# Performance work log

Measured on AMD Instinct MI355X. Metric: run time of the kernel, lower is better.

## Reference

```python
import jax, jax.numpy as jnp
import numpy as np
from jax import lax

N_NODES = 16384
N_EDGES = 262144
T = 64
F_IN = 8
H1, C1 = 12, 16          # globals H and O in the source
HID2 = H1 * C1           # 192, input to second GATConv
LSTM_H = 128
TRAIN_LEN = 32
TARGET_ID = 0
NEG_SLOPE = 0.2


def setup_inputs() -> dict:
    key = jax.random.key(0)
    ks = jax.random.split(key, 16)
    x = jax.random.normal(ks[0], (T, N_NODES, F_IN), jnp.float32)
    src = jax.random.randint(ks[1], (T, N_EDGES), 0, N_NODES)
    dst = jax.random.randint(ks[2], (T, N_EDGES), 0, N_NODES)
    dst = jnp.where(dst == src, (dst + 1) % N_NODES, dst)  # guarantee no self-loops
    edge_index = jnp.stack([src, dst], axis=1)  # (T, 2, E)
    g = lambda k, sh: jax.random.normal(k, sh, jnp.float32) * 0.1
    return {
        "x": x, "edge_index": edge_index,
        "Wl1": g(ks[3], (F_IN, H1 * C1)),
        "att_l1": g(ks[4], (1, H1, C1)), "att_r1": g(ks[5], (1, H1, C1)),
        "b1": jnp.zeros((H1 * C1,), jnp.float32),
        "Wl2": g(ks[6], (HID2, 1)),
        "att_l2": g(ks[7], (1, 1, 1)), "att_r2": g(ks[8], (1, 1, 1)),
        "b2": jnp.zeros((1,), jnp.float32),
        "Wih0": g(ks[9], (4 * LSTM_H, 1)), "Whh0": g(ks[10], (4 * LSTM_H, LSTM_H)),
        "bih0": jnp.zeros((4 * LSTM_H,), jnp.float32), "bhh0": jnp.zeros((4 * LSTM_H,), jnp.float32),
        "Wih1": g(ks[11], (4 * LSTM_H, LSTM_H)), "Whh1": g(ks[12], (4 * LSTM_H, LSTM_H)),
        "bih1": jnp.zeros((4 * LSTM_H,), jnp.float32), "bhh1": jnp.zeros((4 * LSTM_H,), jnp.float32),
        "Wlin": g(ks[13], (1, LSTM_H)), "blin": jnp.zeros((1,), jnp.float32),
    }


def _gat(x, ei, W, att_l, att_r, b, heads, outc, concat):
    N = x.shape[0]
    xl = (x @ W).reshape(N, heads, outc)              # (N,H,C)
    al = jnp.sum(xl * att_l, axis=-1)                 # (N,H)
    ar = jnp.sum(xl * att_r, axis=-1)                 # (N,H)
    loop = jnp.arange(N)
    src = jnp.concatenate([ei[0], loop])              # add self loops (inputs have none)
    dst = jnp.concatenate([ei[1], loop])
    alpha = jax.nn.leaky_relu(al[src] + ar[dst], NEG_SLOPE)  # (E+N, H)
    # segment softmax over destination neighborhoods
    amax = jax.ops.segment_max(alpha, dst, num_segments=N)
    ex = jnp.exp(alpha - amax[dst])
    alpha = ex / (jax.ops.segment_sum(ex, dst, num_segments=N)[dst] + 1e-16)
    # hardcoded per-edge-row edits from message(): s and v copies, then blend
    s = alpha.at[jnp.array([1, 2, 12, 19, 22])].set(0.0).at[jnp.array([7, 14])].set(1.0)
    v = alpha.at[jnp.array([10, 13])].set(0.5).at[jnp.array([17])].set(0.0)
    alpha = 0.8 * alpha + 0.1 * s + 0.1 * v
    out = jax.ops.segment_sum(xl[src] * alpha[:, :, None], dst, num_segments=N)  # (N,H,C)
    out = out.reshape(N, heads * outc) if concat else out.mean(axis=1)
    return out + b


def _lstm_layer(xs, Wih, Whh, bih, bhh):
    # xs: (L, B, in) -> hs: (L, B, H); torch gate order i,f,g,o
    Bsz, Hd = xs.shape[1], Whh.shape[1]
    def step(carry, xt):
        h, c = carry
        gates = xt @ Wih.T + h @ Whh.T + bih + bhh
        i, f, g, o = jnp.split(gates, 4, axis=-1)
        c = jax.nn.sigmoid(f) * c + jax.nn.sigmoid(i) * jnp.tanh(g)
        h = jax.nn.sigmoid(o) * jnp.tanh(c)
        return (h, c), h
    init = (jnp.zeros((Bsz, Hd), xs.dtype), jnp.zeros((Bsz, Hd), xs.dtype))
    _, hs = lax.scan(step, init, xs)
    return hs


def reference(x, edge_index, Wl1, att_l1, att_r1, b1, Wl2, att_l2, att_r2, b2,
              Wih0, Whh0, bih0, bhh0, Wih1, Whh1, bih1, bhh1, Wlin, blin):
    def per_t(args):
        xt, eit = args
        h = _gat(xt, eit, Wl1, att_l1, att_r1, b1, H1, C1, True)
        h = jax.nn.elu(h)
        h = _gat(h, eit, Wl2, att_l2, att_r2, b2, 1, 1, False)
        return h[:, 0]
    out = lax.map(per_t, (x, edge_index))             # (T, N) == xs_out
    series = lax.stop_gradient(out[:, TARGET_ID])     # split_sequences detaches
    idx = jnp.arange(T - TRAIN_LEN)[:, None] + jnp.arange(TRAIN_LEN)[None, :]
    ts = series[idx][:, :, None]                      # (B, L, 1), batch_first
    xs = jnp.transpose(ts, (1, 0, 2))                 # (L, B, 1)
    hs = _lstm_layer(xs, Wih0, Whh0, bih0, bhh0)
    hs = _lstm_layer(hs, Wih1, Whh1, bih1, bhh1)
    return hs[-1] @ Wlin.T + blin                     # (B, 1)
```

## Files before the change

### kernel.cpp

```cpp
#include <hip/hip_runtime.h>
#include <math.h>

#define T 64
#define NN 16384
#define NE 262144
#define FIN 8
#define H1H 12
#define C1C 16
#define HID 192
#define CAP2 95
#define SCAP 96
#define DEGCAP 127
#define LH 128
#define G4 512
#define NB 32
#define NL 32

#define DEV __device__ __forceinline__

DEV float wave_max(float v){
  #pragma unroll
  for (int m = 32; m; m >>= 1) v = fmaxf(v, __shfl_xor(v, m));
  return v;
}
DEV float wave_sum(float v){
  #pragma unroll
  for (int m = 32; m; m >>= 1) v += __shfl_xor(v, m);
  return v;
}
DEV float leaky(float x){ return x >= 0.f ? x : 0.2f * x; }
DEV float sigmoidf(float x){ return 1.f / (1.f + expf(-x)); }

DEV float apply_edit(float a, int eid){
  if (eid >= 32) return a;
  const unsigned m09 = (1u<<1)|(1u<<2)|(1u<<7)|(1u<<10)|(1u<<12)|(1u<<13)|(1u<<14)|(1u<<17)|(1u<<19)|(1u<<22);
  const unsigned mp1 = (1u<<7)|(1u<<14);
  const unsigned mp05 = (1u<<10)|(1u<<13);
  unsigned b = 1u << eid;
  float r = (m09 & b) ? 0.9f * a : a;
  if (mp1 & b) r += 0.1f;
  if (mp05 & b) r += 0.05f;
  return r;
}

__global__ __launch_bounds__(256) void k_scan0(const int* __restrict__ ei,
                                               int* __restrict__ cnt2, int* __restrict__ list2){
  long long gid = (long long)blockIdx.x * blockDim.x + threadIdx.x;
  long long e4 = gid * 4;
  int t = (int)(e4 >> 18);
  int e = (int)(e4 & (NE - 1));
  const int* dstp = ei + (size_t)t * 2 * NE + NE + e;
  int4 d = *(const int4*)dstp;
  int dd[4] = {d.x, d.y, d.z, d.w};
  #pragma unroll
  for (int q = 0; q < 4; q++){
    if (dd[q] == 0){
      int pos = atomicAdd(&cnt2[t], 1);
      if (pos < CAP2) list2[t * CAP2 + pos] = e + q;
    }
  }
}

__global__ __launch_bounds__(128) void k_build(const int* __restrict__ ei, const int* __restrict__ cnt2,
                                               const int* __restrict__ list2, int* __restrict__ scnt,
                                               int* __restrict__ Slist, int* __restrict__ slot_of){
  int t = blockIdx.x;
  int* so = slot_of + (size_t)t * NN;
  int m = min(cnt2[t], CAP2);
  for (int i = threadIdx.x; i < m + 1; i += blockDim.x){
    int u = (i == m) ? 0 : ei[(size_t)t * 2 * NE + list2[t * CAP2 + i]];
    int old = atomicCAS(&so[u], -1, -2);
    if (old == -1){
      int s = atomicAdd(&scnt[t], 1);
      Slist[t * SCAP + s] = u;
      __hip_atomic_store(&so[u], s, __ATOMIC_RELAXED, __HIP_MEMORY_SCOPE_AGENT);
    }
  }
}

__global__ __launch_bounds__(256) void k_scan1(const int* __restrict__ ei, const int* __restrict__ slot_of,
                                               int* __restrict__ ecnt1, int* __restrict__ elist1){
  long long gid = (long long)blockIdx.x * blockDim.x + threadIdx.x;
  long long e4 = gid * 4;
  int t = (int)(e4 >> 18);
  int e = (int)(e4 & (NE - 1));
  const int* dstp = ei + (size_t)t * 2 * NE + NE + e;
  int4 d = *(const int4*)dstp;
  int dd[4] = {d.x, d.y, d.z, d.w};
  #pragma unroll
  for (int q = 0; q < 4; q++){
    int sl = slot_of[(size_t)t * NN + dd[q]];
    if (sl >= 0){
      int pos = atomicAdd(&ecnt1[t * SCAP + sl], 1);
      if (pos < DEGCAP) elist1[((size_t)t * SCAP + sl) * DEGCAP + pos] = e + q;
    }
  }
}

__global__ __launch_bounds__(64, 4) void k_gat1(const float* __restrict__ x, const int* __restrict__ ei,
                                             const float* __restrict__ Wl1, const float* __restrict__ attl,
                                             const float* __restrict__ attr, const float* __restrict__ b1,
                                             const int* __restrict__ scnt, const int* __restrict__ Slist,
                                             const int* __restrict__ ecnt1, const int* __restrict__ elist1,
                                             float* __restrict__ h1){
  int t = blockIdx.y, s = blockIdx.x, h = blockIdx.z;
  if (s >= scnt[t]) return;
  int lane = threadIdx.x;
  int u = Slist[t * SCAP + s];
  int deg = min(ecnt1[t * SCAP + s], DEGCAP);
  int tot = deg + 1;
  bool two = tot > 64;
  const float* xt = x + (size_t)t * NN * FIN;
  const int* srcp = ei + (size_t)t * 2 * NE;
  const int* el = elist1 + ((size_t)t * SCAP + s) * DEGCAP;

  float4 xu_a = ((const float4*)(xt + (size_t)u * FIN))[0];
  float4 xu_b = ((const float4*)(xt + (size_t)u * FIN))[1];
  float xu[FIN] = {xu_a.x, xu_a.y, xu_a.z, xu_a.w, xu_b.x, xu_b.y, xu_b.z, xu_b.w};

  bool act0 = lane < tot;
  int eid0 = 1 << 29;
  int su0 = u;
  if (lane < deg){ int e = el[lane]; eid0 = e; su0 = srcp[e]; }
  float4 xs0a = ((const float4*)(xt + (size_t)su0 * FIN))[0];
  float4 xs0b = ((const float4*)(xt + (size_t)su0 * FIN))[1];
  float xsrc0[FIN] = {xs0a.x, xs0a.y, xs0a.z, xs0a.w, xs0b.x, xs0b.y, xs0b.z, xs0b.w};

  bool act1 = false; int eid1 = 1 << 29;
  float xsrc1[FIN];
  if (two){
    int idx = 64 + lane;
    act1 = idx < tot;
    int su1 = u;
    if (idx < deg){ int e = el[idx]; eid1 = e; su1 = srcp[e]; }
    float4 xs1a = ((const float4*)(xt + (size_t)su1 * FIN))[0];
    float4 xs1b = ((const float4*)(xt + (size_t)su1 * FIN))[1];
    #pragma unroll
    for (int f = 0; f < 4; f++) xsrc1[f] = (&xs1a.x)[f];
    #pragma unroll
    for (int f = 0; f < 4; f++) xsrc1[4 + f] = (&xs1b.x)[f];
  }

  const float* Wh = Wl1 + h * C1C;
  const float* attlh = attl + h * C1C;
  const float* attrh = attr + h * C1C;

  float ar = 0.f;
  #pragma unroll
  for (int c = 0; c < C1C; c++){
    float v = 0.f;
    #pragma unroll
    for (int f = 0; f < FIN; f++) v = fmaf(xu[f], Wh[f * HID + c], v);
    ar = fmaf(v, attrh[c], ar);
  }

  float xls0[C1C];
  float al0 = 0.f;
  #pragma unroll
  for (int c = 0; c < C1C; c++){
    float v = 0.f;
    #pragma unroll
    for (int f = 0; f < FIN; f++) v = fmaf(xsrc0[f], Wh[f * HID + c], v);
    xls0[c] = v;
    al0 = fmaf(v, attlh[c], al0);
  }
  float raw0 = act0 ? leaky(al0 + ar) : -INFINITY;

  float xls1[C1C];
  float raw1 = -INFINITY;
  if (two){
    float al1 = 0.f;
    #pragma unroll
    for (int c = 0; c < C1C; c++){
      float v = 0.f;
      #pragma unroll
      for (int f = 0; f < FIN; f++) v = fmaf(xsrc1[f], Wh[f * HID + c], v);
      xls1[c] = v;
      al1 = fmaf(v, attlh[c], al1);
    }
    raw1 = act1 ? leaky(al1 + ar) : -INFINITY;
  }

  float M = wave_max(fmaxf(raw0, raw1));
  float ex0 = act0 ? expf(raw0 - M) : 0.f;
  float ex1 = act1 ? expf(raw1 - M) : 0.f;
  float S = wave_sum(ex0 + ex1);
  float den = S + 1e-16f;
  float alpha0 = apply_edit(ex0 / den, eid0);
  float alpha1 = two ? apply_edit(ex1 / den, eid1) : 0.f;

  float sum[C1C];
  #pragma unroll
  for (int c = 0; c < C1C; c++){
    sum[c] = xls0[c] * alpha0;
    if (two) sum[c] = fmaf(xls1[c], alpha1, sum[c]);
  }
  #pragma unroll
  for (int m = 32; m; m >>= 1){
    #pragma unroll
    for (int c = 0; c < C1C; c++) sum[c] += __shfl_xor(sum[c], m);
  }
  if (lane == 0){
    float* h1p = h1 + ((size_t)t * SCAP + s) * HID + h * C1C;
    #pragma unroll
    for (int c = 0; c < C1C; c++){
      float v = sum[c] + b1[h * C1C + c];
      h1p[c] = v > 0.f ? v : expm1f(v);
    }
  }
}

__global__ __launch_bounds__(64) void k_gat2(const int* __restrict__ ei, const float* __restrict__ Wl2,
                                             const float* __restrict__ attl2_, const float* __restrict__ attr2_,
                                             const float* __restrict__ b2, const int* __restrict__ cnt2,
                                             const int* __restrict__ list2, const int* __restrict__ slot_of,
                                             const float* __restrict__ h1, float* __restrict__ series){
  int t = blockIdx.x; int lane = threadIdx.x;
  int deg = min(cnt2[t], CAP2);
  int tot = deg + 1;
  const int* srcp = ei + (size_t)t * 2 * NE;
  const int* so = slot_of + (size_t)t * NN;
  float attl2 = attl2_[0], attr2 = attr2_[0];
  int sl0 = so[0];
  const float* h1t = h1 + (size_t)t * SCAP * HID;

  float x0 = 0.f;
  for (int k = 0; k < HID; k++) x0 += h1t[(size_t)sl0 * HID + k] * Wl2[k];

  bool act[2]; int eid[2]; float xl2[2];
  #pragma unroll
  for (int ch = 0; ch < 2; ch++){
    int idx = ch * 64 + lane;
    act[ch] = idx < tot;
    eid[ch] = 1 << 29;
    int sl = sl0;
    if (idx < deg){ int e = list2[t * CAP2 + idx]; eid[ch] = e; sl = so[srcp[e]]; }
    float v = 0.f;
    if (act[ch]) for (int k = 0; k < HID; k++) v += h1t[(size_t)sl * HID + k] * Wl2[k];
    xl2[ch] = v;
  }
  float raw[2];
  #pragma unroll
  for (int ch = 0; ch < 2; ch++) raw[ch] = act[ch] ? leaky(attl2 * xl2[ch] + attr2 * x0) : -INFINITY;
  float M = wave_max(fmaxf(raw[0], raw[1]));
  float ex[2];
  #pragma unroll
  for (int ch = 0; ch < 2; ch++) ex[ch] = act[ch] ? expf(raw[ch] - M) : 0.f;
  float S = wave_sum(ex[0] + ex[1]);
  float den = S + 1e-16f;
  float contrib = apply_edit(ex[0] / den, eid[0]) * xl2[0] + apply_edit(ex[1] / den, eid[1]) * xl2[1];
  contrib = wave_sum(contrib);
  if (lane == 0) series[t] = contrib + b2[0];
}

#define AT_LOADR(p)    __hip_atomic_load((p), __ATOMIC_RELAXED, __HIP_MEMORY_SCOPE_AGENT)
#define AT_STORER(p,v) __hip_atomic_store((p), (v), __ATOMIC_RELAXED, __HIP_MEMORY_SCOPE_AGENT)

#define REP32(M) M(0)M(1)M(2)M(3)M(4)M(5)M(6)M(7)M(8)M(9)M(10)M(11)M(12)M(13)M(14)M(15)\
                 M(16)M(17)M(18)M(19)M(20)M(21)M(22)M(23)M(24)M(25)M(26)M(27)M(28)M(29)M(30)M(31)
#define WDECL(i) float4 w##i;
#define WLOAD(i) w##i = Wr[i];
#define WPIN(i)  asm volatile("" : "+v"(w##i.x), "+v"(w##i.y), "+v"(w##i.z), "+v"(w##i.w));
#define WFMA(i)  { float4 hv = h4[i]; a0 = fmaf(w##i.x, hv.x, a0); a1 = fmaf(w##i.y, hv.y, a1); \
                   a2 = fmaf(w##i.z, hv.z, a2); a3 = fmaf(w##i.w, hv.w, a3); }

__global__ __launch_bounds__(512, 2) void k_lstm(const float* __restrict__ series,
    const float* __restrict__ Wih0, const float* __restrict__ Whh0,
    const float* __restrict__ bih0, const float* __restrict__ bhh0,
    const float* __restrict__ Wih1, const float* __restrict__ Whh1,
    const float* __restrict__ bih1, const float* __restrict__ bhh1,
    const float* __restrict__ Wlin, const float* __restrict__ blin,
    float* __restrict__ h0g, float* __restrict__ xpart,
    int* __restrict__ flagA, int* __restrict__ flagB, float* __restrict__ out){
  int j = threadIdx.x;
  int st = blockIdx.x >> 5;
  int b = blockIdx.x & 31;
  __shared__ __align__(16) float h_lds[LH];
  __shared__ __align__(16) float c_lds[LH];
  __shared__ float gate_lds[G4];
  __shared__ float s_series[NL];
  __shared__ int rdy_lds;
  const float4* h4 = (const float4*)h_lds;

  if (st == 0){
    const float4* Wr = (const float4*)(Whh0 + (size_t)j * LH);
    REP32(WDECL)
    REP32(WLOAD)
    REP32(WPIN)
    float wih = Wih0[j];
    float bsum = bih0[j] + bhh0[j];
    if (j < LH){ h_lds[j] = 0.f; c_lds[j] = 0.f; }
    if (j < NL) s_series[j] = series[b + j];
    __syncthreads();
    for (int t = 0; t < NL; t++){
      float a0 = 0.f, a1 = 0.f, a2 = 0.f, a3 = 0.f;
      REP32(WFMA)
      float acc = fmaf(wih, s_series[t], bsum) + (a0 + a1) + (a2 + a3);
      gate_lds[j] = acc;
      __syncthreads();
      if (j < LH){
        float ig = sigmoidf(gate_lds[j]);
        float fg = sigmoidf(gate_lds[LH + j]);
        float gg = tanhf(gate_lds[2 * LH + j]);
        float og = sigmoidf(gate_lds[3 * LH + j]);
        float c = fg * c_lds[j] + ig * gg;
        float h = og * tanhf(c);
        c_lds[j] = c; h_lds[j] = h;
        AT_STORER(&h0g[(b * NL + t) * LH + j], h);
      }
      __syncthreads();
      if (j == 0) AT_STORER(&flagA[b], t + 1);
    }
  } else if (st == 1){
    const float4* Wr = (const float4*)(Wih1 + (size_t)j * LH);
    REP32(WDECL)
    REP32(WLOAD)
    REP32(WPIN)
    int ready = 0;
    for (int t = 0; t < NL; t++){
      if (ready <= t){
        if (j == 0){
          int f;
          while ((f = AT_LOADR(&flagA[b])) < t + 1) __builtin_amdgcn_s_sleep(1);
          rdy_lds = f;
        }
        __syncthreads();
        ready = rdy_lds;
      }
      if (j < LH) h_lds[j] = AT_LOADR(&h0g[(b * NL + t) * LH + j]);
      __syncthreads();
      float a0 = 0.f, a1 = 0.f, a2 = 0.f, a3 = 0.f;
      REP32(WFMA)
      AT_STORER(&xpart[(b * NL + t) * G4 + j], (a0 + a1) + (a2 + a3));
      __syncthreads();
      if (j == 0) AT_STORER(&flagB[b], t + 1);
    }
  } else {
    const float4* Wr = (const float4*)(Whh1 + (size_t)j * LH);
    REP32(WDECL)
    REP32(WLOAD)
    REP32(WPIN)
    float bsum = bih1[j] + bhh1[j];
    if (j < LH){ h_lds[j] = 0.f; c_lds[j] = 0.f; }
    __syncthreads();
    int ready = 0;
    for (int t = 0; t < NL; t++){
      if (ready <= t){
        if (j == 0){
          int f;
          while ((f = AT_LOADR(&flagB[b])) < t + 1) __builtin_amdgcn_s_sleep(1);
          rdy_lds = f;
        }
        __syncthreads();
        ready = rdy_lds;
      }
      float xj = AT_LOADR(&xpart[(b * NL + t) * G4 + j]);
      float a0 = 0.f, a1 = 0.f, a2 = 0.f, a3 = 0.f;
      REP32(WFMA)
      float acc = xj + bsum + (a0 + a1) + (a2 + a3);
      gate_lds[j] = acc;
      __syncthreads();
      if (j < LH){
        float ig = sigmoidf(gate_lds[j]);
        float fg = sigmoidf(gate_lds[LH + j]);
        float gg = tanhf(gate_lds[2 * LH + j]);
        float og = sigmoidf(gate_lds[3 * LH + j]);
        float c = fg * c_lds[j] + ig * gg;
        float h = og * tanhf(c);
        c_lds[j] = c; h_lds[j] = h;
      }
      __syncthreads();
    }
    if (j == 0){
      float s2 = blin[0];
      for (int k = 0; k < LH; k++) s2 += Wlin[k] * h_lds[k];
      out[b] = s2;
    }
  }
}

extern "C" void kernel_launch(void* const* d_in, const int* in_sizes, int n_in,
                              void* d_out, int out_size, void* d_ws, size_t ws_size,
                              hipStream_t stream) {
  const float* x     = (const float*)d_in[0];
  const int*   ei    = (const int*)  d_in[1];
  const float* Wl1   = (const float*)d_in[2];
  const float* attl1 = (const float*)d_in[3];
  const float* attr1 = (const float*)d_in[4];
  const float* b1    = (const float*)d_in[5];
  const float* Wl2   = (const float*)d_in[6];
  const float* attl2 = (const float*)d_in[7];
  const float* attr2 = (const float*)d_in[8];
  const float* b2    = (const float*)d_in[9];
  const float* Wih0  = (const float*)d_in[10];
  const float* Whh0  = (const float*)d_in[11];
  const float* bih0  = (const float*)d_in[12];
  const float* bhh0  = (const float*)d_in[13];
  const float* Wih1  = (const float*)d_in[14];
  const float* Whh1  = (const float*)d_in[15];
  const float* bih1  = (const float*)d_in[16];
  const float* bhh1  = (const float*)d_in[17];
  const float* Wlin  = (const float*)d_in[18];
  const float* blin  = (const float*)d_in[19];
  float* out = (float*)d_out;

  char* wsb = (char*)d_ws;
  size_t off = 0;
  auto alloc = [&](size_t bytes)->void*{
    void* p = wsb + off;
    off += (bytes + 255) & ~(size_t)255;
    return p;
  };
  int* cnt2  = (int*)alloc(T * 4);
  int* scnt  = (int*)alloc(T * 4);
  int* ecnt1 = (int*)alloc(T * SCAP * 4);
  int* flagA = (int*)alloc(NB * 4);
  int* flagB = (int*)alloc(NB * 4);
  size_t ctrl_bytes = off;
  int* slot_of = (int*)alloc((size_t)T * NN * 4);
  int* list2   = (int*)alloc((size_t)T * CAP2 * 4);
  int* Slist   = (int*)alloc((size_t)T * SCAP * 4);
  int* elist1  = (int*)alloc((size_t)T * SCAP * DEGCAP * 4);
  float* h1    = (float*)alloc((size_t)T * SCAP * HID * 4);
  float* series= (float*)alloc(T * 4);
  float* h0g   = (float*)alloc((size_t)NB * NL * LH * 4);
  float* xpart = (float*)alloc((size_t)NB * NL * G4 * 4);

  hipMemsetAsync(d_ws, 0, ctrl_bytes, stream);
  hipMemsetAsync(slot_of, 0xFF, (size_t)T * NN * 4, stream);

  k_scan0<<<T * NE / 4 / 256, 256, 0, stream>>>(ei, cnt2, list2);
  k_build<<<T, 128, 0, stream>>>(ei, cnt2, list2, scnt, Slist, slot_of);
  k_scan1<<<T * NE / 4 / 256, 256, 0, stream>>>(ei, slot_of, ecnt1, elist1);
  k_gat1<<<dim3(SCAP, T, H1H), 64, 0, stream>>>(x, ei, Wl1, attl1, attr1, b1, scnt, Slist, ecnt1, elist1, h1);
  k_gat2<<<T, 64, 0, stream>>>(ei, Wl2, attl2, attr2, b2, cnt2, list2, slot_of, h1, series);
  k_lstm<<<96, 512, 0, stream>>>(series, Wih0, Whh0, bih0, bhh0, Wih1, Whh1, bih1, bhh1,
                                 Wlin, blin, h0g, xpart, flagA, flagB, out);
}
```

Before: 415.7 us.

## Split LSTM gate dot products across two thread halves with LDS reduction

The LSTM kernel now launches 1024 threads per block instead of 512. Each gate row's 128-long dot product is split between two threads that each hold half the weights in registers, and the two partial sums are reduced through shared memory. This halves the serial FMA chain and the register pressure per thread. In exchange it adds an extra barrier and LDS round trip per timestep, and the flag polling no longer caches readiness ahead of time.

```diff
diff --git a/kernel.cpp b/kernel.cpp
--- a/kernel.cpp
+++ b/kernel.cpp
@@ -256,15 +256,14 @@
 #define AT_LOADR(p)    __hip_atomic_load((p), __ATOMIC_RELAXED, __HIP_MEMORY_SCOPE_AGENT)
 #define AT_STORER(p,v) __hip_atomic_store((p), (v), __ATOMIC_RELAXED, __HIP_MEMORY_SCOPE_AGENT)
 
-#define REP32(M) M(0)M(1)M(2)M(3)M(4)M(5)M(6)M(7)M(8)M(9)M(10)M(11)M(12)M(13)M(14)M(15)\
-                 M(16)M(17)M(18)M(19)M(20)M(21)M(22)M(23)M(24)M(25)M(26)M(27)M(28)M(29)M(30)M(31)
+#define REP16(M) M(0)M(1)M(2)M(3)M(4)M(5)M(6)M(7)M(8)M(9)M(10)M(11)M(12)M(13)M(14)M(15)
 #define WDECL(i) float4 w##i;
 #define WLOAD(i) w##i = Wr[i];
 #define WPIN(i)  asm volatile("" : "+v"(w##i.x), "+v"(w##i.y), "+v"(w##i.z), "+v"(w##i.w));
-#define WFMA(i)  { float4 hv = h4[i]; a0 = fmaf(w##i.x, hv.x, a0); a1 = fmaf(w##i.y, hv.y, a1); \
+#define WFMA(i)  { float4 hv = h4h[i]; a0 = fmaf(w##i.x, hv.x, a0); a1 = fmaf(w##i.y, hv.y, a1); \
                    a2 = fmaf(w##i.z, hv.z, a2); a3 = fmaf(w##i.w, hv.w, a3); }
 
-__global__ __launch_bounds__(512, 2) void k_lstm(const float* __restrict__ series,
+__global__ __launch_bounds__(1024, 4) void k_lstm(const float* __restrict__ series,
     const float* __restrict__ Wih0, const float* __restrict__ Whh0,
     const float* __restrict__ bih0, const float* __restrict__ bhh0,
     const float* __restrict__ Wih1, const float* __restrict__ Whh1,
@@ -272,106 +271,102 @@
     const float* __restrict__ Wlin, const float* __restrict__ blin,
     float* __restrict__ h0g, float* __restrict__ xpart,
     int* __restrict__ flagA, int* __restrict__ flagB, float* __restrict__ out){
-  int j = threadIdx.x;
+  int tid = threadIdx.x;
   int st = blockIdx.x >> 5;
   int b = blockIdx.x & 31;
+  int row = tid & 511;
+  int half = tid >> 9;
   __shared__ __align__(16) float h_lds[LH];
-  __shared__ __align__(16) float c_lds[LH];
-  __shared__ float gate_lds[G4];
+  __shared__ float c_lds[LH];
+  __shared__ float part[1024];
   __shared__ float s_series[NL];
-  __shared__ int rdy_lds;
   const float4* h4 = (const float4*)h_lds;
 
   if (st == 0){
-    const float4* Wr = (const float4*)(Whh0 + (size_t)j * LH);
-    REP32(WDECL)
-    REP32(WLOAD)
-    REP32(WPIN)
-    float wih = Wih0[j];
-    float bsum = bih0[j] + bhh0[j];
-    if (j < LH){ h_lds[j] = 0.f; c_lds[j] = 0.f; }
-    if (j < NL) s_series[j] = series[b + j];
+    const float4* Wr = (const float4*)(Whh0 + (size_t)row * LH) + half * 16;
+    REP16(WDECL)
+    REP16(WLOAD)
+    REP16(WPIN)
+    float wih = Wih0[row];
+    float bsum = bih0[row] + bhh0[row];
+    if (tid < LH){ h_lds[tid] = 0.f; c_lds[tid] = 0.f; }
+    if (tid < NL) s_series[tid] = series[b + tid];
     __syncthreads();
     for (int t = 0; t < NL; t++){
+      const float4* h4h = h4 + half * 16;
       float a0 = 0.f, a1 = 0.f, a2 = 0.f, a3 = 0.f;
-      REP32(WFMA)
-      float acc = fmaf(wih, s_series[t], bsum) + (a0 + a1) + (a2 + a3);
-      gate_lds[j] = acc;
-      __syncthreads();
-      if (j < LH){
-        float ig = sigmoidf(gate_lds[j]);
-        float fg = sigmoidf(gate_lds[LH + j]);
-        float gg = tanhf(gate_lds[2 * LH + j]);
-        float og = sigmoidf(gate_lds[3 * LH + j]);
-        float c = fg * c_lds[j] + ig * gg;
+      REP16(WFMA)
+      part[tid] = (a0 + a1) + (a2 + a3);
+      __syncthreads();
+      if (tid < G4) part[tid] = part[tid] + part[tid + G4] + fmaf(wih, s_series[t], bsum);
+      __syncthreads();
+      if (tid < LH){
+        float ig = sigmoidf(part[tid]);
+        float fg = sigmoidf(part[LH + tid]);
+        float gg = tanhf(part[2 * LH + tid]);
+        float og = sigmoidf(part[3 * LH + tid]);
+        float c = fg * c_lds[tid] + ig * gg;
         float h = og * tanhf(c);
-        c_lds[j] = c; h_lds[j] = h;
-        AT_STORER(&h0g[(b * NL + t) * LH + j], h);
+        c_lds[tid] = c; h_lds[tid] = h;
+        AT_STORER(&h0g[(b * NL + t) * LH + tid], h);
       }
       __syncthreads();
-      if (j == 0) AT_STORER(&flagA[b], t + 1);
+      if (tid == 0) AT_STORER(&flagA[b], t + 1);
     }
   } else if (st == 1){
-    const float4* Wr = (const float4*)(Wih1 + (size_t)j * LH);
-    REP32(WDECL)
-    REP32(WLOAD)
-    REP32(WPIN)
-    int ready = 0;
+    const float4* Wr = (const float4*)(Wih1 + (size_t)row * LH) + half * 16;
+    REP16(WDECL)
+    REP16(WLOAD)
+    REP16(WPIN)
     for (int t = 0; t < NL; t++){
-      if (ready <= t){
-        if (j == 0){
-          int f;
-          while ((f = AT_LOADR(&flagA[b])) < t + 1) __builtin_amdgcn_s_sleep(1);
-          rdy_lds = f;
-        }
-        __syncthreads();
-        ready = rdy_lds;
+      if (tid == 0){
+        while (AT_LOADR(&flagA[b]) < t + 1) __builtin_amdgcn_s_sleep(1);
       }
-      if (j < LH) h_lds[j] = AT_LOADR(&h0g[(b * NL + t) * LH + j]);
-      __syncthreads();
+      __syncthreads();
+      if (tid < LH) h_lds[tid] = AT_LOADR(&h0g[(b * NL + t) * LH + tid]);
+      __syncthreads();
+      const float4* h4h = h4 + half * 16;
       float a0 = 0.f, a1 = 0.f, a2 = 0.f, a3 = 0.f;
-      REP32(WFMA)
-      AT_STORER(&xpart[(b * NL + t) * G4 + j], (a0 + a1) + (a2 + a3));
-      __syncthreads();
-      if (j == 0) AT_STORER(&flagB[b], t + 1);
+      REP16(WFMA)
+      part[tid] = (a0 + a1) + (a2 + a3);
+      __syncthreads();
+      if (tid < G4) AT_STORER(&xpart[(b * NL + t) * G4 + tid], part[tid] + part[tid + G4]);
+      __syncthreads();
+      if (tid == 0) AT_STORER(&flagB[b], t + 1);
     }
   } else {
-    const float4* Wr = (const float4*)(Whh1 + (size_t)j * LH);
-    REP32(WDECL)
-    REP32(WLOAD)
-    REP32(WPIN)
-    float bsum = bih1[j] + bhh1[j];
-    if (j < LH){ h_lds[j] = 0.f; c_lds[j] = 0.f; }
+    const float4* Wr = (const float4*)(Whh1 + (size_t)row * LH) + half * 16;
+    REP16(WDECL)
+    REP16(WLOAD)
+    REP16(WPIN)
+    float bsum = bih1[row] + bhh1[row];
+    if (tid < LH){ h_lds[tid] = 0.f; c_lds[tid] = 0.f; }
     __syncthreads();
-    int ready = 0;
     for (int t = 0; t < NL; t++){
-      if (ready <= t){
-        if (j == 0){
-          int f;
-          while ((f = AT_LOADR(&flagB[b])) < t + 1) __builtin_amdgcn_s_sleep(1);
-          rdy_lds = f;
-        }
-        __syncthreads();
-        ready = rdy_lds;
+      if (tid == 0){
+        while (AT_LOADR(&flagB[b]) < t + 1) __builtin_amdgcn_s_sleep(1);
       }
-      float xj = AT_LOADR(&xpart[(b * NL + t) * G4 + j]);
+      __syncthreads();
+      const float4* h4h = h4 + half * 16;
       float a0 = 0.f, a1 = 0.f, a2 = 0.f, a3 = 0.f;
-      REP32(WFMA)
-      float acc = xj + bsum + (a0 + a1) + (a2 + a3);
-      gate_lds[j] = acc;
-      __syncthreads();
-      if (j < LH){
-        float ig = sigmoidf(gate_lds[j]);
-        float fg = sigmoidf(gate_lds[LH + j]);
-        float gg = tanhf(gate_lds[2 * LH + j]);
-        float og = sigmoidf(gate_lds[3 * LH + j]);
-        float c = fg * c_lds[j] + ig * gg;
+      REP16(WFMA)
+      float xj = (tid < G4) ? AT_LOADR(&xpart[(b * NL + t) * G4 + tid]) : 0.f;
+      part[tid] = (a0 + a1) + (a2 + a3);
+      __syncthreads();
+      if (tid < G4) part[tid] = part[tid] + part[tid + G4] + xj + bsum;
+      __syncthreads();
+      if (tid < LH){
+        float ig = sigmoidf(part[tid]);
+        float fg = sigmoidf(part[LH + tid]);
+        float gg = tanhf(part[2 * LH + tid]);
+        float og = sigmoidf(part[3 * LH + tid]);
+        float c = fg * c_lds[tid] + ig * gg;
         float h = og * tanhf(c);
-        c_lds[j] = c; h_lds[j] = h;
+        c_lds[tid] = c; h_lds[tid] = h;
       }
       __syncthreads();
     }
-    if (j == 0){
+    if (tid == 0){
       float s2 = blin[0];
       for (int k = 0; k < LH; k++) s2 += Wlin[k] * h_lds[k];
       out[b] = s2;
@@ -434,6 +429,6 @@
   k_scan1<<<T * NE / 4 / 256, 256, 0, stream>>>(ei, slot_of, ecnt1, elist1);
   k_gat1<<<dim3(SCAP, T, H1H), 64, 0, stream>>>(x, ei, Wl1, attl1, attr1, b1, scnt, Slist, ecnt1, elist1, h1);
   k_gat2<<<T, 64, 0, stream>>>(ei, Wl2, attl2, attr2, b2, cnt2, list2, slot_of, h1, series);
-  k_lstm<<<96, 512, 0, stream>>>(series, Wih0, Whh0, bih0, bhh0, Wih1, Whh1, bih1, bhh1,
-                                 Wlin, blin, h0g, xpart, flagA, flagB, out);
-}
+  k_lstm<<<96, 1024, 0, stream>>>(series, Wih0, Whh0, bih0, bhh0, Wih1, Whh1, bih1, bhh1,
+                                  Wlin, blin, h0g, xpart, flagA, flagB, out);
+}
```

Measured after the change: 519.1 us. 1.25x slower.
